# Kernel tuning notes

Measured on AMD Instinct MI355X. Metric: run time of the kernel, lower is better.

The kernel has to match this reference:

```python
import jax, jax.numpy as jnp
import numpy as np

N = 100_000      # num nodes
E = 1_600_000    # num edges
DIN, H, L, NQ = 3, 64, 5, 50_000
BN_EPS = 1e-5


def setup_inputs() -> dict:
    key = jax.random.key(0)
    ks = jax.random.split(key, 24)
    f = lambda k, s, sc=1.0: jax.random.normal(k, s, dtype=jnp.float32) * sc
    inv = 1.0 / np.sqrt(H)
    return {
        "x": f(ks[0], (N, DIN)),
        "edge_index": jax.random.randint(ks[1], (2, E), 0, N, dtype=jnp.int32),
        "n_qubits": NQ,
        "w_in": f(ks[2], (DIN, H), 0.5),
        "b_in": f(ks[3], (H,), 0.1),
        "msg_w1": f(ks[4], (L, H, H), inv),
        "msg_b1": f(ks[5], (L, H), 0.1),
        "msg_w2": f(ks[6], (L, H, H), inv),
        "msg_b2": f(ks[7], (L, H), 0.1),
        "upd_w1": f(ks[8], (L, 2 * H, H), 1.0 / np.sqrt(2 * H)),
        "upd_b1": f(ks[9], (L, H), 0.1),
        "upd_w2": f(ks[10], (L, H, H), inv),
        "upd_b2": f(ks[11], (L, H), 0.1),
        "bn_g": jax.random.uniform(ks[12], (L, H), jnp.float32, 0.5, 1.5),
        "bn_b": f(ks[13], (L, H), 0.1),
        "bn_m": f(ks[14], (L, H), 0.1),
        "bn_v": jax.random.uniform(ks[15], (L, H), jnp.float32, 0.5, 1.5),
        "out_w1": f(ks[16], (H, H // 2), inv),
        "out_b1": f(ks[17], (H // 2,), 0.1),
        "out_w2": f(ks[18], (H // 2, 1), 1.0 / np.sqrt(H // 2)),
        "out_b2": f(ks[19], (1,), 0.1),
    }


def reference(x, edge_index, n_qubits, w_in, b_in,
              msg_w1, msg_b1, msg_w2, msg_b2,
              upd_w1, upd_b1, upd_w2, upd_b2,
              bn_g, bn_b, bn_m, bn_v,
              out_w1, out_b1, out_w2, out_b2):
    src, dst = edge_index[0], edge_index[1]  # PyG: x_j = x[src], aggregate at dst
    h = jax.nn.relu(x @ w_in + b_in)         # [N, H]
    for i in range(L):
        xj = h[src]                                                    # gather [E, H]
        m = jax.nn.relu(xj @ msg_w1[i] + msg_b1[i]) @ msg_w2[i] + msg_b2[i]
        agg = jax.ops.segment_sum(m, dst, num_segments=N)              # scatter-add [N, H]
        comb = jnp.concatenate([h, agg], axis=-1)                      # [N, 2H]
        hn = jax.nn.relu(comb @ upd_w1[i] + upd_b1[i]) @ upd_w2[i] + upd_b2[i]
        # BatchNorm1d (eval mode: running stats) + residual + relu (dropout=eval identity)
        hn = (hn - bn_m[i]) * jax.lax.rsqrt(bn_v[i] + BN_EPS) * bn_g[i] + bn_b[i]
        h = jax.nn.relu(hn + h)
    q = h[:n_qubits]                                                   # qubit nodes [NQ, H]
    return jax.nn.relu(q @ out_w1 + out_b1) @ out_w2 + out_b2          # [NQ, 1]
```

## Files before the change

kernel.cpp:

```cpp
#include <hip/hip_runtime.h>
#include <hip/hip_bf16.h>

#define H 64
#define PADW 88
#define PADT 68
#define CAP 10240
#define WSTRIDE 20480

typedef __attribute__((ext_vector_type(8))) short short8;
typedef __attribute__((ext_vector_type(4))) short short4v;
typedef __attribute__((ext_vector_type(4))) float floatx4;

#define MFMA(a, b, c) __builtin_amdgcn_mfma_f32_16x16x32_bf16(a, b, c, 0, 0, 0)

__device__ __forceinline__ float bf2f(short s) {
  union { unsigned int u; float f; } v;
  v.u = ((unsigned int)(unsigned short)s) << 16;
  return v.f;
}
__device__ __forceinline__ short f2bf(float f) {
  union { float f; unsigned int u; } v; v.f = f;
  unsigned int r = v.u + 0x7fffu + ((v.u >> 16) & 1u);
  return (short)(r >> 16);
}
__device__ __forceinline__ void split2(float v, short& hi, short& lo) {
  hi = f2bf(v);
  lo = f2bf(v - bf2f(hi));
}
__device__ __forceinline__ float ldf(const void* p, long idx, bool isf32) {
  return isf32 ? ((const float*)p)[idx] : bf2f(((const short*)p)[idx]);
}

__global__ void k_probe(const short* __restrict__ x, int* __restrict__ flag) {
  __shared__ int cnt;
  if (threadIdx.x == 0) cnt = 0;
  __syncthreads();
  short s = x[threadIdx.x];
  int e = (s >> 7) & 0xFF;
  int insane = (e != 0 && (e < 100 || e > 140)) ? 1 : 0;
  atomicAdd(&cnt, insane);
  __syncthreads();
  if (threadIdx.x == 0) *flag = (cnt > 64) ? 1 : 0;
}

__global__ void k_input2(const void* __restrict__ x, const void* __restrict__ w,
                         const void* __restrict__ b, short* __restrict__ hhi,
                         short* __restrict__ hlo, const int* __restrict__ flag, int N) {
  bool isf32 = (*flag != 0);
  int idx = blockIdx.x * 256 + threadIdx.x;
  if (idx >= N * H) return;
  int v = idx >> 6, k = idx & 63;
  float acc = ldf(b, k, isf32);
#pragma unroll
  for (int d = 0; d < 3; ++d)
    acc += ldf(x, (long)v * 3 + d, isf32) * ldf(w, d * 64 + k, isf32);
  float r = fmaxf(acc, 0.f);
  short hi, lo; split2(r, hi, lo);
  hhi[idx] = hi; hlo[idx] = lo;
}

__global__ void k_prep(const void* __restrict__ U1, const void* __restrict__ U2,
                       const void* __restrict__ W1m, const void* __restrict__ W2m,
                       short* __restrict__ prep, const int* __restrict__ flag) {
  bool isf32 = (*flag != 0);
  int i = blockIdx.x;
  short* p = prep + (long)i * WSTRIDE;
  long oU = (long)i * 8192, oW = (long)i * 4096;
  for (int idx = threadIdx.x; idx < 8192; idx += 256) {
    int in = idx >> 6, n = idx & 63;
    int t = n >> 4, mm = n & 15, c = in >> 5, qq = (in >> 3) & 3, jj = in & 7;
    p[(((t * 4 + c) * 64) + (qq * 16 + mm)) * 8 + jj] = f2bf(ldf(U1, oU + idx, isf32));
  }
  for (int idx = threadIdx.x; idx < 4096; idx += 256) {
    int in = idx >> 6, n = idx & 63;
    int t = n >> 4, mm = n & 15, c = in >> 5, qq = (in >> 3) & 3, jj = in & 7;
    int fi = (((t * 2 + c) * 64) + (qq * 16 + mm)) * 8 + jj;
    p[8192 + fi]  = f2bf(ldf(U2, oW + idx, isf32));
    p[12288 + fi] = f2bf(ldf(W1m, oW + idx, isf32));
    p[16384 + fi] = f2bf(ldf(W2m, oW + idx, isf32));
  }
}


__global__ void k_bcount(const int* __restrict__ dstI, int* __restrict__ bcnt, int E) {
  __shared__ int cl[1024];
  int tid = threadIdx.x;
  for (int t = tid; t < 1024; t += 256) cl[t] = 0;
  __syncthreads();
  for (int i = blockIdx.x * 256 + tid; i < E; i += gridDim.x * 256)
    atomicAdd(&cl[dstI[i] >> 8], 1);
  __syncthreads();
  for (int t = tid; t < 1024; t += 256)
    if (cl[t]) atomicAdd(&bcnt[t], cl[t]);
}

__global__ void k_bscan(const int* __restrict__ bcnt, int* __restrict__ bbase,
                        int* __restrict__ bcur) {
  __shared__ int s[256];
  int tid = threadIdx.x;
  int base = tid * 4;
  int v0 = bcnt[base], v1 = bcnt[base + 1], v2 = bcnt[base + 2], v3 = bcnt[base + 3];
  int tsum = v0 + v1 + v2 + v3;
  s[tid] = tsum;
  __syncthreads();
  for (int off = 1; off < 256; off <<= 1) {
    int x = (tid >= off) ? s[tid - off] : 0;
    __syncthreads();
    s[tid] += x;
    __syncthreads();
  }
  int excl = s[tid] - tsum;
  bbase[base] = excl;           bcur[base] = excl;
  bbase[base + 1] = excl + v0;  bcur[base + 1] = excl + v0;
  bbase[base + 2] = excl + v0 + v1;      bcur[base + 2] = excl + v0 + v1;
  bbase[base + 3] = excl + v0 + v1 + v2; bcur[base + 3] = excl + v0 + v1 + v2;
  if (tid == 255) bbase[1024] = s[255];
}

__global__ void k_bin(const int* __restrict__ srcI, const int* __restrict__ dstI,
                      int* __restrict__ bcur, int2* __restrict__ pairs, int E) {
  __shared__ int cl[1024], cur[1024];
  int tid = threadIdx.x;
  int chunk = (E + gridDim.x - 1) / gridDim.x;
  int s = blockIdx.x * chunk;
  int e = min(s + chunk, E);
  for (int t = tid; t < 1024; t += 256) cl[t] = 0;
  __syncthreads();
  for (int i = s + tid; i < e; i += 256) atomicAdd(&cl[dstI[i] >> 8], 1);
  __syncthreads();
  for (int t = tid; t < 1024; t += 256)
    cur[t] = cl[t] ? atomicAdd(&bcur[t], cl[t]) : 0;
  __syncthreads();
  for (int i = s + tid; i < e; i += 256) {
    int d = dstI[i];
    int p = atomicAdd(&cur[d >> 8], 1);
    pairs[p] = (int2){srcI[i], d};
  }
}

__global__ __launch_bounds__(256) void k_sortb(
    const int2* __restrict__ pairs, const int* __restrict__ bbase,
    int* __restrict__ rowptr, int* __restrict__ srcS, int N, int E, int B) {
  __shared__ int cnt[256], cur[256], s2[256];
  __shared__ int stage[CAP];
  int b = blockIdx.x, tid = threadIdx.x;
  int lo = b << 8;
  int W = min(256, N - lo);
  int s = bbase[b], e = bbase[b + 1];
  cnt[tid] = 0;
  __syncthreads();
  for (int i = s + tid; i < e; i += 256)
    atomicAdd(&cnt[pairs[i].y - lo], 1);
  __syncthreads();
  int v = (tid < W) ? cnt[tid] : 0;
  s2[tid] = v;
  __syncthreads();
  for (int off = 1; off < 256; off <<= 1) {
    int x = (tid >= off) ? s2[tid - off] : 0;
    __syncthreads();
    s2[tid] += x;
    __syncthreads();
  }
  int excl = s2[tid] - v;
  if (tid < W) {
    rowptr[lo + tid] = s + excl;
    cur[tid] = excl;
  }
  if (b == B - 1 && tid == 0) rowptr[N] = E;
  __syncthreads();
  for (int i = s + tid; i < e; i += 256) {
    int2 pr = pairs[i];
    int p = atomicAdd(&cur[pr.y - lo], 1);
    if (p < CAP) stage[p] = pr.x;
    else srcS[s + p] = pr.x;
  }
  __syncthreads();
  int Sb = e - s;
  int lim = Sb < CAP ? Sb : CAP;
  for (int i = tid; i < lim; i += 256) srcS[s + i] = stage[i];
}

__global__ __launch_bounds__(256) void k_mlp(
    const short* __restrict__ hhi, const short* __restrict__ hlo,
    const void* __restrict__ W1, const void* __restrict__ B1,
    const void* __restrict__ W2, long oW, long oB,
    short* __restrict__ M, const int* __restrict__ flag, int N) {
  __shared__ short w1hi[64 * PADW], w1lo[64 * PADW];
  __shared__ short w2hi[64 * PADW], w2lo[64 * PADW];
  __shared__ float b1s[64];
  __shared__ float tbuf[4][16 * PADT];

  bool isf32 = (*flag != 0);
  int tid = threadIdx.x;
  for (int idx = tid; idx < 4096; idx += 256) {
    int j = idx >> 6, k = idx & 63;
    short hi, lo;
    split2(ldf(W1, oW + idx, isf32), hi, lo);
    w1hi[k * PADW + j] = hi; w1lo[k * PADW + j] = lo;
    split2(ldf(W2, oW + idx, isf32), hi, lo);
    w2hi[k * PADW + j] = hi; w2lo[k * PADW + j] = lo;
  }
  if (tid < 64) b1s[tid] = ldf(B1, oB + tid, isf32);
  __syncthreads();

  const int wave = tid >> 6, lane = tid & 63;
  const int m = lane & 15, quad = lane >> 4;
  float* tb = tbuf[wave];

  for (int nb = blockIdx.x * 64; nb < N; nb += gridDim.x * 64) {
    const int nBase = nb + wave * 16;
    int node = nBase + m;
    int nc = node < N ? node : N - 1;

    short8 fhi[2], flo[2];
    fhi[0] = *(const short8*)(hhi + (long)nc * H + quad * 8);
    fhi[1] = *(const short8*)(hhi + (long)nc * H + 32 + quad * 8);
    flo[0] = *(const short8*)(hlo + (long)nc * H + quad * 8);
    flo[1] = *(const short8*)(hlo + (long)nc * H + 32 + quad * 8);

    floatx4 acc[4];
#pragma unroll
    for (int t = 0; t < 4; ++t) acc[t] = (floatx4){0.f, 0.f, 0.f, 0.f};
#pragma unroll
    for (int t = 0; t < 4; ++t) {
      const short* whi = &w1hi[(t * 16 + m) * PADW + quad * 8];
      const short* wlo = &w1lo[(t * 16 + m) * PADW + quad * 8];
      acc[t] = MFMA(fhi[0], *(const short8*)(whi), acc[t]);
      acc[t] = MFMA(fhi[1], *(const short8*)(whi + 32), acc[t]);
      acc[t] = MFMA(flo[0], *(const short8*)(whi), acc[t]);
      acc[t] = MFMA(flo[1], *(const short8*)(whi + 32), acc[t]);
      acc[t] = MFMA(fhi[0], *(const short8*)(wlo), acc[t]);
      acc[t] = MFMA(fhi[1], *(const short8*)(wlo + 32), acc[t]);
    }

#pragma unroll
    for (int t = 0; t < 4; ++t) {
      int col = t * 16 + m;
      float bb = b1s[col];
#pragma unroll
      for (int r = 0; r < 4; ++r)
        tb[(quad * 4 + r) * PADT + col] = fmaxf(acc[t][r] + bb, 0.f);
    }

    float av[16];
    *(floatx4*)(av + 0)  = *(const floatx4*)(&tb[m * PADT + quad * 8]);
    *(floatx4*)(av + 4)  = *(const floatx4*)(&tb[m * PADT + quad * 8 + 4]);
    *(floatx4*)(av + 8)  = *(const floatx4*)(&tb[m * PADT + 32 + quad * 8]);
    *(floatx4*)(av + 12) = *(const floatx4*)(&tb[m * PADT + 32 + quad * 8 + 4]);
    short8 thi0, tlo0, thi1, tlo1;
#pragma unroll
    for (int j = 0; j < 8; ++j) {
      short hi, lo;
      split2(av[j], hi, lo);     thi0[j] = hi; tlo0[j] = lo;
      split2(av[8 + j], hi, lo); thi1[j] = hi; tlo1[j] = lo;
    }

    floatx4 mac[4];
#pragma unroll
    for (int t = 0; t < 4; ++t) mac[t] = (floatx4){0.f, 0.f, 0.f, 0.f};
#pragma unroll
    for (int t = 0; t < 4; ++t) {
      const short* whi = &w2hi[(t * 16 + m) * PADW + quad * 8];
      const short* wlo = &w2lo[(t * 16 + m) * PADW + quad * 8];
      mac[t] = MFMA(thi0, *(const short8*)(whi), mac[t]);
      mac[t] = MFMA(thi1, *(const short8*)(whi + 32), mac[t]);
      mac[t] = MFMA(tlo0, *(const short8*)(whi), mac[t]);
      mac[t] = MFMA(tlo1, *(const short8*)(whi + 32), mac[t]);
      mac[t] = MFMA(thi0, *(const short8*)(wlo), mac[t]);
      mac[t] = MFMA(thi1, *(const short8*)(wlo + 32), mac[t]);
    }

#pragma unroll
    for (int t = 0; t < 4; ++t) {
      int col = t * 16 + m;
#pragma unroll
      for (int r = 0; r < 4; ++r) {
        int nrow = nBase + quad * 4 + r;
        if (nrow < N) M[(long)nrow * H + col] = f2bf(mac[t][r]);
      }
    }
  }
}

__global__ __launch_bounds__(256) void k_gather(
    const short* __restrict__ M, const int* __restrict__ rowptr,
    const int* __restrict__ srcS, const void* __restrict__ B2, long oB,
    short* __restrict__ agg, const int* __restrict__ flag, int N, int totWaves) {
  __shared__ float b2s[64];
  bool isf32 = (*flag != 0);
  if (threadIdx.x < 64) b2s[threadIdx.x] = ldf(B2, oB + threadIdx.x, isf32);
  __syncthreads();
  const int wave = threadIdx.x >> 6, lane = threadIdx.x & 63;
  const int g = lane >> 4, l = lane & 15;
  float b2v[4];
#pragma unroll
  for (int j = 0; j < 4; ++j) b2v[j] = b2s[l * 4 + j];

  const int gw = blockIdx.x * 4 + wave;
  const int nTask = (N + 3) >> 2;
  for (int task = gw; task < nTask; task += totWaves) {
    int n = task * 4 + g;
    bool valid = n < N;
    int nc = valid ? n : N - 1;
    int rs = rowptr[nc], re = rowptr[nc + 1];
    if (!valid) { rs = 0; re = 0; }
    float a0 = 0.f, a1 = 0.f, a2 = 0.f, a3 = 0.f;
    for (int e = rs; e < re; e += 8) {
      int sv[8];
#pragma unroll
      for (int u = 0; u < 8; ++u) {
        int c = e + u < re ? e + u : re - 1;
        sv[u] = srcS[c];
      }
      short4v rr[8];
#pragma unroll
      for (int u = 0; u < 8; ++u)
        rr[u] = *(const short4v*)(M + (long)sv[u] * H + l * 4);
#pragma unroll
      for (int u = 0; u < 8; ++u) {
        if (e + u < re) {
          a0 += bf2f(rr[u][0]); a1 += bf2f(rr[u][1]);
          a2 += bf2f(rr[u][2]); a3 += bf2f(rr[u][3]);
        }
      }
    }
    if (valid) {
      float dv = (float)(re - rs);
      short4v o;
      o[0] = f2bf(a0 + dv * b2v[0]);
      o[1] = f2bf(a1 + dv * b2v[1]);
      o[2] = f2bf(a2 + dv * b2v[2]);
      o[3] = f2bf(a3 + dv * b2v[3]);
      *(short4v*)(agg + (long)n * H + l * 4) = o;
    }
  }
}

__global__ __launch_bounds__(256) void k_updm(
    short* __restrict__ hhi, short* __restrict__ hlo, const short* __restrict__ agg,
    const short* __restrict__ pw, const short* __restrict__ pwn,
    const void* __restrict__ UB1, const void* __restrict__ UB2,
    const void* __restrict__ G, const void* __restrict__ Bb,
    const void* __restrict__ Mm, const void* __restrict__ Vv,
    const void* __restrict__ B1m,
    long oB, long oBn,
    short* __restrict__ Mout, const int* __restrict__ flag, int N, int doMsg) {
  __shared__ short u1f[8192];
  __shared__ short u2f[4096];
  __shared__ short m1f[4096];
  __shared__ float b1s[64], b2s[64], scl[64], sft[64], mb1[64];
  __shared__ float tbuf[4][16 * PADT];

  bool isf32 = (*flag != 0);
  int tid = threadIdx.x;
  const int wave = tid >> 6, lane = tid & 63;
  const int m = lane & 15, quad = lane >> 4;

  for (int c = tid; c < 1024; c += 256)
    ((short8*)u1f)[c] = ((const short8*)pw)[c];
  for (int c = tid; c < 512; c += 256) {
    ((short8*)u2f)[c] = ((const short8*)(pw + 8192))[c];
    ((short8*)m1f)[c] = ((const short8*)(pwn + 12288))[c];
  }
  short8 m2r[4][2];
#pragma unroll
  for (int t = 0; t < 4; ++t)
#pragma unroll
    for (int c = 0; c < 2; ++c)
      m2r[t][c] = *(const short8*)&pwn[16384 + (((t * 2 + c) * 64) + lane) * 8];
  if (tid < 64) {
    b1s[tid] = ldf(UB1, oB + tid, isf32);
    b2s[tid] = ldf(UB2, oB + tid, isf32);
    float s = ldf(G, oB + tid, isf32) * rsqrtf(ldf(Vv, oB + tid, isf32) + 1e-5f);
    scl[tid] = s;
    sft[tid] = ldf(Bb, oB + tid, isf32) - ldf(Mm, oB + tid, isf32) * s;
    mb1[tid] = ldf(B1m, oBn + tid, isf32);
  }
  __syncthreads();

  float* tb = tbuf[wave];

  for (int nb = blockIdx.x * 64; nb < N; nb += gridDim.x * 64) {
    const int nBase = nb + wave * 16;
    int node = nBase + m;
    int nc = node < N ? node : N - 1;

    short8 fhi[4], flo[2];
    fhi[0] = *(const short8*)(hhi + (long)nc * H + quad * 8);
    fhi[1] = *(const short8*)(hhi + (long)nc * H + 32 + quad * 8);
    flo[0] = *(const short8*)(hlo + (long)nc * H + quad * 8);
    flo[1] = *(const short8*)(hlo + (long)nc * H + 32 + quad * 8);
    fhi[2] = *(const short8*)(agg + (long)nc * H + quad * 8);
    fhi[3] = *(const short8*)(agg + (long)nc * H + 32 + quad * 8);

    floatx4 acc[4];
#pragma unroll
    for (int t = 0; t < 4; ++t) acc[t] = (floatx4){0.f, 0.f, 0.f, 0.f};
#pragma unroll
    for (int t = 0; t < 4; ++t) {
#pragma unroll
      for (int c = 0; c < 4; ++c) {
        const short8 w = *(const short8*)&u1f[(((t * 4 + c) * 64) + lane) * 8];
        acc[t] = MFMA(fhi[c], w, acc[t]);
        if (c < 2) acc[t] = MFMA(flo[c], w, acc[t]);
      }
    }

#pragma unroll
    for (int t = 0; t < 4; ++t) {
      int col = t * 16 + m;
      float bb = b1s[col];
#pragma unroll
      for (int r = 0; r < 4; ++r)
        tb[(quad * 4 + r) * PADT + col] = fmaxf(acc[t][r] + bb, 0.f);
    }
    float av[16];
    *(floatx4*)(av + 0)  = *(const floatx4*)(&tb[m * PADT + quad * 8]);
    *(floatx4*)(av + 4)  = *(const floatx4*)(&tb[m * PADT + quad * 8 + 4]);
    *(floatx4*)(av + 8)  = *(const floatx4*)(&tb[m * PADT + 32 + quad * 8]);
    *(floatx4*)(av + 12) = *(const floatx4*)(&tb[m * PADT + 32 + quad * 8 + 4]);
    short8 thi[2], tlo[2];
#pragma unroll
    for (int j = 0; j < 8; ++j) {
      short hi, lo;
      split2(av[j], hi, lo);     thi[0][j] = hi; tlo[0][j] = lo;
      split2(av[8 + j], hi, lo); thi[1][j] = hi; tlo[1][j] = lo;
    }

    floatx4 mac[4];
#pragma unroll
    for (int t = 0; t < 4; ++t) mac[t] = (floatx4){0.f, 0.f, 0.f, 0.f};
#pragma unroll
    for (int t = 0; t < 4; ++t) {
#pragma unroll
      for (int c = 0; c < 2; ++c) {
        const short8 w = *(const short8*)&u2f[(((t * 2 + c) * 64) + lane) * 8];
        mac[t] = MFMA(thi[c], w, mac[t]);
        mac[t] = MFMA(tlo[c], w, mac[t]);
      }
    }

#pragma unroll
    for (int t = 0; t < 4; ++t) {
      int col = t * 16 + m;
      float bb = b2s[col], ss = scl[col], ff = sft[col];
#pragma unroll
      for (int r = 0; r < 4; ++r) {
        int nrow = nBase + quad * 4 + r;
        float hn = 0.f;
        if (nrow < N) {
          long el = (long)nrow * H + col;
          float hv = (mac[t][r] + bb) * ss + ff;
          float ho = bf2f(hhi[el]) + bf2f(hlo[el]);
          hn = fmaxf(hv + ho, 0.f);
          short hi2, lo2; split2(hn, hi2, lo2);
          hhi[el] = hi2; hlo[el] = lo2;
        }
        tb[(quad * 4 + r) * PADT + col] = hn;
      }
    }

    if (doMsg) {
      *(floatx4*)(av + 0)  = *(const floatx4*)(&tb[m * PADT + quad * 8]);
      *(floatx4*)(av + 4)  = *(const floatx4*)(&tb[m * PADT + quad * 8 + 4]);
      *(floatx4*)(av + 8)  = *(const floatx4*)(&tb[m * PADT + 32 + quad * 8]);
      *(floatx4*)(av + 12) = *(const floatx4*)(&tb[m * PADT + 32 + quad * 8 + 4]);
#pragma unroll
      for (int j = 0; j < 8; ++j) {
        short hi, lo;
        split2(av[j], hi, lo);     thi[0][j] = hi; tlo[0][j] = lo;
        split2(av[8 + j], hi, lo); thi[1][j] = hi; tlo[1][j] = lo;
      }

#pragma unroll
      for (int t = 0; t < 4; ++t) acc[t] = (floatx4){0.f, 0.f, 0.f, 0.f};
#pragma unroll
      for (int t = 0; t < 4; ++t) {
#pragma unroll
        for (int c = 0; c < 2; ++c) {
          const short8 w = *(const short8*)&m1f[(((t * 2 + c) * 64) + lane) * 8];
          acc[t] = MFMA(thi[c], w, acc[t]);
          acc[t] = MFMA(tlo[c], w, acc[t]);
        }
      }

#pragma unroll
      for (int t = 0; t < 4; ++t) {
        int col = t * 16 + m;
        float bb = mb1[col];
#pragma unroll
        for (int r = 0; r < 4; ++r)
          tb[(quad * 4 + r) * PADT + col] = fmaxf(acc[t][r] + bb, 0.f);
      }
      *(floatx4*)(av + 0)  = *(const floatx4*)(&tb[m * PADT + quad * 8]);
      *(floatx4*)(av + 4)  = *(const floatx4*)(&tb[m * PADT + quad * 8 + 4]);
      *(floatx4*)(av + 8)  = *(const floatx4*)(&tb[m * PADT + 32 + quad * 8]);
      *(floatx4*)(av + 12) = *(const floatx4*)(&tb[m * PADT + 32 + quad * 8 + 4]);
#pragma unroll
      for (int j = 0; j < 8; ++j) {
        short hi, lo;
        split2(av[j], hi, lo);     thi[0][j] = hi; tlo[0][j] = lo;
        split2(av[8 + j], hi, lo); thi[1][j] = hi; tlo[1][j] = lo;
      }

#pragma unroll
      for (int t = 0; t < 4; ++t) mac[t] = (floatx4){0.f, 0.f, 0.f, 0.f};
#pragma unroll
      for (int t = 0; t < 4; ++t) {
#pragma unroll
        for (int c = 0; c < 2; ++c) {
          mac[t] = MFMA(thi[c], m2r[t][c], mac[t]);
          mac[t] = MFMA(tlo[c], m2r[t][c], mac[t]);
        }
      }

#pragma unroll
      for (int t = 0; t < 4; ++t) {
        int col = t * 16 + m;
#pragma unroll
        for (int r = 0; r < 4; ++r) {
          int nrow = nBase + quad * 4 + r;
          if (nrow < N) Mout[(long)nrow * H + col] = f2bf(mac[t][r]);
        }
      }
    }
  }
}

__global__ __launch_bounds__(256) void k_out2(
    const short* __restrict__ hhi, const short* __restrict__ hlo,
    const void* __restrict__ W1, const void* __restrict__ B1,
    const void* __restrict__ W2, const void* __restrict__ B2,
    void* __restrict__ out, const int* __restrict__ flag, int NQ) {
  __shared__ float w1s[64 * 32];
  __shared__ float b1sh[32], w2s[32];
  bool isf32 = (*flag != 0);
  int tid = threadIdx.x;
  for (int idx = tid; idx < 2048; idx += 256) w1s[idx] = ldf(W1, idx, isf32);
  if (tid < 32) { b1sh[tid] = ldf(B1, tid, isf32); w2s[tid] = ldf(W2, tid, isf32); }
  __syncthreads();
  int v = blockIdx.x * 256 + tid;
  if (v >= NQ) return;
  float hr[64];
#pragma unroll
  for (int j = 0; j < 64; ++j)
    hr[j] = bf2f(hhi[(long)v * H + j]) + bf2f(hlo[(long)v * H + j]);
  float accum = ldf(B2, 0, isf32);
#pragma unroll 4
  for (int k = 0; k < 32; ++k) {
    float t = b1sh[k];
#pragma unroll
    for (int j = 0; j < 64; ++j) t += hr[j] * w1s[j * 32 + k];
    accum += fmaxf(t, 0.f) * w2s[k];
  }
  if (isf32) ((float*)out)[v] = accum;
  else ((short*)out)[v] = f2bf(accum);
}

extern "C" void kernel_launch(void* const* d_in, const int* in_sizes, int n_in,
                              void* d_out, int out_size, void* d_ws, size_t ws_size,
                              hipStream_t stream) {
  const void* x      = d_in[0];
  const int*  ei     = (const int*)d_in[1];
  const void* w_in   = d_in[3];
  const void* b_in   = d_in[4];
  const void* msg_w1 = d_in[5];
  const void* msg_b1 = d_in[6];
  const void* msg_w2 = d_in[7];
  const void* msg_b2 = d_in[8];
  const void* upd_w1 = d_in[9];
  const void* upd_b1 = d_in[10];
  const void* upd_w2 = d_in[11];
  const void* upd_b2 = d_in[12];
  const void* bn_g   = d_in[13];
  const void* bn_b   = d_in[14];
  const void* bn_m   = d_in[15];
  const void* bn_v   = d_in[16];
  const void* out_w1 = d_in[17];
  const void* out_b1 = d_in[18];
  const void* out_w2 = d_in[19];
  const void* out_b2 = d_in[20];

  const int N = in_sizes[0] / 3;
  const int E = in_sizes[1] / 2;
  const int L = in_sizes[5] / (H * H);
  const int* srcI = ei;
  const int* dstI = ei + E;
  const int B = (N + 255) >> 8;

  size_t off = 0;
  auto alloc = [&](size_t bytes) { size_t o = off; off += (bytes + 255) & ~(size_t)255; return o; };
  size_t mSize = (size_t)N * H * sizeof(short);
  size_t pSize = (size_t)E * sizeof(int2);
  size_t o_flag   = alloc(256);
  size_t o_bcnt   = alloc(1024 * sizeof(int));
  size_t o_bbase  = alloc(1025 * sizeof(int));
  size_t o_bcur   = alloc(1024 * sizeof(int));
  size_t o_prep   = alloc((size_t)L * WSTRIDE * sizeof(short));
  size_t o_hhi    = alloc((size_t)N * H * sizeof(short));
  size_t o_hlo    = alloc((size_t)N * H * sizeof(short));
  size_t o_agg    = alloc((size_t)N * H * sizeof(short));
  size_t o_M      = alloc(mSize > pSize ? mSize : pSize);
  size_t o_rowptr = alloc((size_t)(N + 1) * sizeof(int));
  size_t o_srcS   = alloc((size_t)E * sizeof(int));

  char* ws = (char*)d_ws;
  int*   flag   = (int*)(ws + o_flag);
  int*   bcnt   = (int*)(ws + o_bcnt);
  int*   bbase  = (int*)(ws + o_bbase);
  int*   bcur   = (int*)(ws + o_bcur);
  short* prep   = (short*)(ws + o_prep);
  short* hhi    = (short*)(ws + o_hhi);
  short* hlo    = (short*)(ws + o_hlo);
  short* aggS   = (short*)(ws + o_agg);
  short* Mbuf   = (short*)(ws + o_M);
  int2*  pairs  = (int2*)(ws + o_M);
  int*   rowptr = (int*)(ws + o_rowptr);
  int*   srcS   = (int*)(ws + o_srcS);

  k_probe<<<1, 256, 0, stream>>>((const short*)x, flag);
  k_prep<<<L, 256, 0, stream>>>(upd_w1, upd_w2, msg_w1, msg_w2, prep, flag);
  k_input2<<<(N * H + 255) / 256, 256, 0, stream>>>(x, w_in, b_in, hhi, hlo, flag, N);

  hipMemsetAsync(bcnt, 0, 1024 * sizeof(int), stream);
  k_bcount<<<256, 256, 0, stream>>>(dstI, bcnt, E);
  k_bscan<<<1, 256, 0, stream>>>(bcnt, bbase, bcur);
  k_bin<<<256, 256, 0, stream>>>(srcI, dstI, bcur, pairs, E);
  k_sortb<<<B, 256, 0, stream>>>(pairs, bbase, rowptr, srcS, N, E, B);

  k_mlp<<<768, 256, 0, stream>>>(hhi, hlo,
      msg_w1, msg_b1, msg_w2, 0, 0, Mbuf, flag, N);

  const int GB = 2048;
  const int UB = 768;
  for (int i = 0; i < L; ++i) {
    long oB = (long)i * H;
    int doMsg = (i + 1 < L) ? 1 : 0;
    int iN = doMsg ? i + 1 : i;
    long oBn = doMsg ? (long)(i + 1) * H : 0;
    k_gather<<<GB, 256, 0, stream>>>(Mbuf, rowptr, srcS,
        msg_b2, oB, aggS, flag, N, GB * 4);
    k_updm<<<UB, 256, 0, stream>>>(hhi, hlo, aggS,
        prep + (size_t)i * WSTRIDE, prep + (size_t)iN * WSTRIDE,
        upd_b1, upd_b2, bn_g, bn_b, bn_m, bn_v, msg_b1,
        oB, oBn, Mbuf, flag, N, doMsg);
  }
  k_out2<<<(out_size + 255) / 256, 256, 0, stream>>>(hhi, hlo,
      out_w1, out_b1, out_w2, out_b2, d_out, flag, out_size);
}
```

Before: 548.2 us.

## Fuse CSR gather-aggregation into update kernel with ping-pong message buffers

Removes the separate k_gather kernel and performs each node's neighbor-message sum inside k_updm. Results go into per-wave shared memory tiles and are converted to bf16 MFMA operands there. This avoids writing and re-reading the agg array and saves one launch per layer. Because other blocks now read messages while the next layer's messages are written, two message buffers alternate by layer. The gather now runs at the update kernel's 768-block grid with serial subloops, which may cut the memory-level parallelism available for the random gathers.

```diff
diff --git a/kernel.cpp b/kernel.cpp
--- a/kernel.cpp
+++ b/kernel.cpp
@@ -282,73 +282,21 @@
   }
 }
 
-__global__ __launch_bounds__(256) void k_gather(
-    const short* __restrict__ M, const int* __restrict__ rowptr,
-    const int* __restrict__ srcS, const void* __restrict__ B2, long oB,
-    short* __restrict__ agg, const int* __restrict__ flag, int N, int totWaves) {
-  __shared__ float b2s[64];
-  bool isf32 = (*flag != 0);
-  if (threadIdx.x < 64) b2s[threadIdx.x] = ldf(B2, oB + threadIdx.x, isf32);
-  __syncthreads();
-  const int wave = threadIdx.x >> 6, lane = threadIdx.x & 63;
-  const int g = lane >> 4, l = lane & 15;
-  float b2v[4];
-#pragma unroll
-  for (int j = 0; j < 4; ++j) b2v[j] = b2s[l * 4 + j];
-
-  const int gw = blockIdx.x * 4 + wave;
-  const int nTask = (N + 3) >> 2;
-  for (int task = gw; task < nTask; task += totWaves) {
-    int n = task * 4 + g;
-    bool valid = n < N;
-    int nc = valid ? n : N - 1;
-    int rs = rowptr[nc], re = rowptr[nc + 1];
-    if (!valid) { rs = 0; re = 0; }
-    float a0 = 0.f, a1 = 0.f, a2 = 0.f, a3 = 0.f;
-    for (int e = rs; e < re; e += 8) {
-      int sv[8];
-#pragma unroll
-      for (int u = 0; u < 8; ++u) {
-        int c = e + u < re ? e + u : re - 1;
-        sv[u] = srcS[c];
-      }
-      short4v rr[8];
-#pragma unroll
-      for (int u = 0; u < 8; ++u)
-        rr[u] = *(const short4v*)(M + (long)sv[u] * H + l * 4);
-#pragma unroll
-      for (int u = 0; u < 8; ++u) {
-        if (e + u < re) {
-          a0 += bf2f(rr[u][0]); a1 += bf2f(rr[u][1]);
-          a2 += bf2f(rr[u][2]); a3 += bf2f(rr[u][3]);
-        }
-      }
-    }
-    if (valid) {
-      float dv = (float)(re - rs);
-      short4v o;
-      o[0] = f2bf(a0 + dv * b2v[0]);
-      o[1] = f2bf(a1 + dv * b2v[1]);
-      o[2] = f2bf(a2 + dv * b2v[2]);
-      o[3] = f2bf(a3 + dv * b2v[3]);
-      *(short4v*)(agg + (long)n * H + l * 4) = o;
-    }
-  }
-}
-
 __global__ __launch_bounds__(256) void k_updm(
-    short* __restrict__ hhi, short* __restrict__ hlo, const short* __restrict__ agg,
+    short* __restrict__ hhi, short* __restrict__ hlo,
+    const short* __restrict__ Min, const int* __restrict__ rowptr,
+    const int* __restrict__ srcS,
     const short* __restrict__ pw, const short* __restrict__ pwn,
     const void* __restrict__ UB1, const void* __restrict__ UB2,
     const void* __restrict__ G, const void* __restrict__ Bb,
     const void* __restrict__ Mm, const void* __restrict__ Vv,
-    const void* __restrict__ B1m,
+    const void* __restrict__ B1m, const void* __restrict__ B2m,
     long oB, long oBn,
     short* __restrict__ Mout, const int* __restrict__ flag, int N, int doMsg) {
   __shared__ short u1f[8192];
   __shared__ short u2f[4096];
   __shared__ short m1f[4096];
-  __shared__ float b1s[64], b2s[64], scl[64], sft[64], mb1[64];
+  __shared__ float b1s[64], b2s[64], scl[64], sft[64], mb1[64], mb2[64];
   __shared__ float tbuf[4][16 * PADT];
 
   bool isf32 = (*flag != 0);
@@ -375,10 +323,15 @@
     scl[tid] = s;
     sft[tid] = ldf(Bb, oB + tid, isf32) - ldf(Mm, oB + tid, isf32) * s;
     mb1[tid] = ldf(B1m, oBn + tid, isf32);
+    mb2[tid] = ldf(B2m, oB + tid, isf32);
   }
   __syncthreads();
 
   float* tb = tbuf[wave];
+
+  float b2v[4];
+#pragma unroll
+  for (int j = 0; j < 4; ++j) b2v[j] = mb2[m * 4 + j];
 
   for (int nb = blockIdx.x * 64; nb < N; nb += gridDim.x * 64) {
     const int nBase = nb + wave * 16;
@@ -390,8 +343,57 @@
     fhi[1] = *(const short8*)(hhi + (long)nc * H + 32 + quad * 8);
     flo[0] = *(const short8*)(hlo + (long)nc * H + quad * 8);
     flo[1] = *(const short8*)(hlo + (long)nc * H + 32 + quad * 8);
-    fhi[2] = *(const short8*)(agg + (long)nc * H + quad * 8);
-    fhi[3] = *(const short8*)(agg + (long)nc * H + 32 + quad * 8);
+
+    {
+      const int g = quad, l = m;
+#pragma unroll 1
+      for (int sub = 0; sub < 4; ++sub) {
+        int n = nBase + sub * 4 + g;
+        bool valid = n < N;
+        int ng = valid ? n : N - 1;
+        int rs = rowptr[ng], re = rowptr[ng + 1];
+        if (!valid) { rs = 0; re = 0; }
+        float a0 = 0.f, a1 = 0.f, a2 = 0.f, a3 = 0.f;
+        for (int e = rs; e < re; e += 8) {
+          int sv[8];
+#pragma unroll
+          for (int u = 0; u < 8; ++u) {
+            int c = e + u < re ? e + u : re - 1;
+            sv[u] = srcS[c];
+          }
+          short4v rr[8];
+#pragma unroll
+          for (int u = 0; u < 8; ++u)
+            rr[u] = *(const short4v*)(Min + (long)sv[u] * H + l * 4);
+#pragma unroll
+          for (int u = 0; u < 8; ++u) {
+            if (e + u < re) {
+              a0 += bf2f(rr[u][0]); a1 += bf2f(rr[u][1]);
+              a2 += bf2f(rr[u][2]); a3 += bf2f(rr[u][3]);
+            }
+          }
+        }
+        float dv = (float)(re - rs);
+        float* row = &tb[(sub * 4 + g) * PADT + l * 4];
+        row[0] = a0 + dv * b2v[0];
+        row[1] = a1 + dv * b2v[1];
+        row[2] = a2 + dv * b2v[2];
+        row[3] = a3 + dv * b2v[3];
+      }
+    }
+
+    {
+      float ag[16];
+      *(floatx4*)(ag + 0)  = *(const floatx4*)(&tb[m * PADT + quad * 8]);
+      *(floatx4*)(ag + 4)  = *(const floatx4*)(&tb[m * PADT + quad * 8 + 4]);
+      *(floatx4*)(ag + 8)  = *(const floatx4*)(&tb[m * PADT + 32 + quad * 8]);
+      *(floatx4*)(ag + 12) = *(const floatx4*)(&tb[m * PADT + 32 + quad * 8 + 4]);
+#pragma unroll
+      for (int j = 0; j < 8; ++j) {
+        fhi[2][j] = f2bf(ag[j]);
+        fhi[3][j] = f2bf(ag[8 + j]);
+      }
+    }
 
     floatx4 acc[4];
 #pragma unroll
@@ -599,8 +601,8 @@
   size_t o_prep   = alloc((size_t)L * WSTRIDE * sizeof(short));
   size_t o_hhi    = alloc((size_t)N * H * sizeof(short));
   size_t o_hlo    = alloc((size_t)N * H * sizeof(short));
-  size_t o_agg    = alloc((size_t)N * H * sizeof(short));
-  size_t o_M      = alloc(mSize > pSize ? mSize : pSize);
+  size_t o_MA     = alloc(mSize > pSize ? mSize : pSize);
+  size_t o_MB     = alloc(mSize);
   size_t o_rowptr = alloc((size_t)(N + 1) * sizeof(int));
   size_t o_srcS   = alloc((size_t)E * sizeof(int));
 
@@ -612,9 +614,9 @@
   short* prep   = (short*)(ws + o_prep);
   short* hhi    = (short*)(ws + o_hhi);
   short* hlo    = (short*)(ws + o_hlo);
-  short* aggS   = (short*)(ws + o_agg);
-  short* Mbuf   = (short*)(ws + o_M);
-  int2*  pairs  = (int2*)(ws + o_M);
+  short* MA     = (short*)(ws + o_MA);
+  short* MB     = (short*)(ws + o_MB);
+  int2*  pairs  = (int2*)(ws + o_MA);
   int*   rowptr = (int*)(ws + o_rowptr);
   int*   srcS   = (int*)(ws + o_srcS);
 
@@ -629,21 +631,20 @@
   k_sortb<<<B, 256, 0, stream>>>(pairs, bbase, rowptr, srcS, N, E, B);
 
   k_mlp<<<768, 256, 0, stream>>>(hhi, hlo,
-      msg_w1, msg_b1, msg_w2, 0, 0, Mbuf, flag, N);
-
-  const int GB = 2048;
+      msg_w1, msg_b1, msg_w2, 0, 0, MA, flag, N);
+
   const int UB = 768;
   for (int i = 0; i < L; ++i) {
     long oB = (long)i * H;
     int doMsg = (i + 1 < L) ? 1 : 0;
     int iN = doMsg ? i + 1 : i;
     long oBn = doMsg ? (long)(i + 1) * H : 0;
-    k_gather<<<GB, 256, 0, stream>>>(Mbuf, rowptr, srcS,
-        msg_b2, oB, aggS, flag, N, GB * 4);
-    k_updm<<<UB, 256, 0, stream>>>(hhi, hlo, aggS,
+    const short* Min = (i & 1) ? MB : MA;
+    short*       Mo  = (i & 1) ? MA : MB;
+    k_updm<<<UB, 256, 0, stream>>>(hhi, hlo, Min, rowptr, srcS,
         prep + (size_t)i * WSTRIDE, prep + (size_t)iN * WSTRIDE,
-        upd_b1, upd_b2, bn_g, bn_b, bn_m, bn_v, msg_b1,
-        oB, oBn, Mbuf, flag, N, doMsg);
+        upd_b1, upd_b2, bn_g, bn_b, bn_m, bn_v, msg_b1, msg_b2,
+        oB, oBn, Mo, flag, N, doMsg);
   }
   k_out2<<<(out_size + 255) / 256, 256, 0, stream>>>(hhi, hlo,
       out_w1, out_b1, out_w2, out_b2, d_out, flag, out_size);
```

Result: slower. 679.3 us (+23.9%).
